# Kernel optimization log

Measured on AMD Instinct MI355X. Metric: run time of the kernel, lower is better.

The kernel has to match this reference:

```python
import jax, jax.numpy as jnp
import numpy as np

B, N_PER_G, H, K, A, GNN_STEPS = 64, 100, 64, 5, 50, 3
N = B * N_PER_G  # total nodes


def _lin(key, din, dout):
    s = 1.0 / np.sqrt(din)
    kw, kb = jax.random.split(key)
    w = jax.random.uniform(kw, (din, dout), minval=-s, maxval=s, dtype=jnp.float32)
    b = jax.random.uniform(kb, (dout,), minval=-s, maxval=s, dtype=jnp.float32)
    return w, b


def setup_inputs() -> dict:
    key = jax.random.key(0)
    ks = jax.random.split(key, 16)
    # complete graph (no self loops) per batch graph
    i, j = np.meshgrid(np.arange(N_PER_G), np.arange(N_PER_G), indexing="ij")
    m = i != j
    s0, d0 = i[m], j[m]  # [n*(n-1)]
    offs = (np.arange(B) * N_PER_G)[:, None]
    src = jnp.asarray((s0[None, :] + offs).reshape(-1), dtype=jnp.int32)
    dst = jnp.asarray((d0[None, :] + offs).reshape(-1), dtype=jnp.int32)
    E = src.shape[0]
    e_type = jax.random.uniform(ks[0], (E, 2), dtype=jnp.float32)
    d = jax.random.uniform(ks[1], (E, 1), dtype=jnp.float32)
    label = jax.nn.one_hot(jax.random.randint(ks[2], (N,), 0, K), K, dtype=jnp.float32)
    actions = jax.random.randint(ks[3], (B * A, 2), 0, N_PER_G)
    l1_w, l1_b = _lin(ks[4], K, H)
    l2_w, l2_b = _lin(ks[5], H, H)
    t3_w, t3_b = _lin(ks[6], H, H)
    t4_wf, t4_b = _lin(ks[7], 1, H)
    t5_wf, t5_b = _lin(ks[8], H, 1)
    t6_w, t6_b = _lin(ks[9], H, H)
    t7_1_w, t7_1_b = _lin(ks[10], H, H)
    t7_2_w, t7_2_b = _lin(ks[11], H, H)
    t9_1_w, t9_1_b = _lin(ks[12], H, H)
    t9_2_w, t9_2_b = _lin(ks[13], H, H)
    return dict(label=label, e_type=e_type, d=d,
                l1_w=l1_w, l1_b=l1_b, l2_w=l2_w, l2_b=l2_b,
                t3_w=t3_w, t3_b=t3_b, t4_w=t4_wf[0], t4_b=t4_b,
                t5_w=t5_wf[:, 0], t5_b=t5_b, t6_w=t6_w, t6_b=t6_b,
                t7_1_w=t7_1_w, t7_1_b=t7_1_b, t7_2_w=t7_2_w, t7_2_b=t7_2_b,
                t9_1_w=t9_1_w, t9_1_b=t9_1_b, t9_2_w=t9_2_w, t9_2_b=t9_2_b,
                src=src, dst=dst, actions=actions)


def reference(label, e_type, d, l1_w, l1_b, l2_w, l2_b, t3_w, t3_b, t4_w, t4_b,
              t5_w, t5_b, t6_w, t6_b, t7_1_w, t7_1_b, t7_2_w, t7_2_b,
              t9_1_w, t9_1_b, t9_2_w, t9_2_b, src, dst, actions):
    e1 = e_type[:, 0]
    # n1_hd = h[src]*e1, n1_d = d*e1; bmm(n1_hd^T, n1_d) == sum over in-edges of h[src]*e1^2*d
    w_e = (e1 * e1) * d[:, 0]                              # [E]
    s_e = d[:, 0] * e1                                     # per-edge n1_d scalar [E]
    # sum_deg relu(t4(n1_d)) as edge-parallel relu + scatter-add
    t4_edge = jax.nn.relu(s_e[:, None] * t4_w[None, :] + t4_b)   # [E,H]
    t4_sum = jax.ops.segment_sum(t4_edge, dst, num_segments=N)   # [N,H]
    base = label @ l1_w + l1_b + t4_sum @ t3_w + t3_b            # constant across gnn steps
    h = jnp.zeros((N, H), dtype=label.dtype)
    for _ in range(GNN_STEPS):
        n1_h = jax.ops.segment_sum(h[src] * w_e[:, None], dst, num_segments=N)  # [N,H]
        h = jax.nn.relu(base + n1_h @ l2_w + l2_b)
    # readout (forward_): graph mean -> t6 stem; per-action node-pair branch
    stem = h.reshape(B, N_PER_G, H).mean(axis=1) @ t6_w + t6_b    # [B,H]
    h2 = h @ t7_1_w + t7_1_b                                      # [N,H]
    offs = jnp.repeat(jnp.arange(B, dtype=actions.dtype) * N_PER_G, A)
    a = actions + offs[:, None]                                   # global node ids [B*A,2]
    ha = h2[a[:, 0]] + h2[a[:, 1]]                                # [B*A,H]
    u = jax.nn.relu(jax.nn.relu(ha) @ t7_2_w + t7_2_b) @ t9_2_w + t9_2_b
    g_branch = jax.nn.relu(stem) @ t9_1_w + t9_1_b                # [B,H]
    q = jax.nn.relu(g_branch[:, None, :] + u.reshape(B, A, H))    # [B,A,H]
    Q_sa = q.reshape(B * A, H) @ t5_w + t5_b[0]                   # [B*A]
    return Q_sa
```

## Files before the change

kernel.cpp:

```cpp
#include <hip/hip_runtime.h>

#define HD 64
#define NPG 100
#define NGRP 64
#define NACT 50
#define EPG 9900

typedef const float* fcp;

__global__ __launch_bounds__(512)
void k_edge_base(fcp label, fcp e_type, fcp dvec,
                 fcp l1_w, fcp l1_b, fcp l2_b,
                 fcp t3_w, fcp t3_b, fcp t4_w, fcp t4_b,
                 float* __restrict__ Wt, float* __restrict__ baseo,
                 float* __restrict__ hA)
{
    const int g  = blockIdx.x >> 2;
    const int c  = blockIdx.x & 3;
    const int j0 = c * 25;
    const int t  = threadIdx.x;
    const int hh = t & 63;
    const int w  = t >> 6;

    __shared__ __align__(16) float s_ld[2500];
    __shared__ __align__(16) float w_ld[2500];
    __shared__ __align__(16) float t4s[25 * HD];

    float lab[4][5], l1r[5];
    #pragma unroll
    for (int kk = 0; kk < 5; ++kk) l1r[kk] = l1_w[kk * HD + hh];
    #pragma unroll
    for (int m = 0; m < 4; ++m) {
        const int jl = w + 8 * m;
        #pragma unroll
        for (int kk = 0; kk < 5; ++kk)
            lab[m][kk] = (jl < 25) ? label[(g * NPG + j0 + jl) * 5 + kk] : 0.f;
    }

    const float2* et2 = (const float2*)e_type;
    const int ebase = g * EPG;
    for (int idx = t; idx < 2500; idx += 512) {
        const int i  = idx / 25;
        const int jl = idx - i * 25;
        const int j  = j0 + jl;
        float s = 0.f, wv = 0.f;
        if (i != j) {
            const int e = ebase + i * 99 + j - (j > i ? 1 : 0);
            const float e1 = et2[e].x;
            const float dd = dvec[e];
            s  = dd * e1;
            wv = e1 * e1 * dd;
        }
        s_ld[jl * 100 + i] = s;
        w_ld[jl * 100 + i] = wv;
    }
    __syncthreads();

    {
        float* wd = Wt + g * (NPG * NPG) + j0 * NPG;
        for (int idx = t; idx < 2500; idx += 512) wd[idx] = w_ld[idx];
    }

    const float w4  = t4_w[hh];
    const float b4  = t4_b[hh];
    const float rb4 = fmaxf(b4, 0.f);
    #pragma unroll
    for (int m = 0; m < 4; ++m) {
        const int jl = w + 8 * m;
        if (jl < 25) {
            float a0 = 0.f, a1 = 0.f, a2 = 0.f, a3 = 0.f;
            #pragma unroll 5
            for (int ib = 0; ib < 25; ++ib) {
                const float4 s4 = *(const float4*)&s_ld[jl * 100 + 4 * ib];
                a0 += fmaxf(s4.x * w4 + b4, 0.f);
                a1 += fmaxf(s4.y * w4 + b4, 0.f);
                a2 += fmaxf(s4.z * w4 + b4, 0.f);
                a3 += fmaxf(s4.w * w4 + b4, 0.f);
            }
            t4s[jl * HD + hh] = (a0 + a1) + (a2 + a3) - rb4;
        }
    }

    const float bb   = l1_b[hh] + t3_b[hh];
    const float l2bv = l2_b[hh];
    float v[4];
    #pragma unroll
    for (int m = 0; m < 4; ++m) {
        float x = bb;
        #pragma unroll
        for (int kk = 0; kk < 5; ++kk) x += lab[m][kk] * l1r[kk];
        v[m] = x;
    }
    for (int ib = 0; ib < 16; ++ib) {
        const float tw0 = t3_w[(4 * ib + 0) * HD + hh];
        const float tw1 = t3_w[(4 * ib + 1) * HD + hh];
        const float tw2 = t3_w[(4 * ib + 2) * HD + hh];
        const float tw3 = t3_w[(4 * ib + 3) * HD + hh];
        #pragma unroll
        for (int m = 0; m < 4; ++m) {
            const int jl = w + 8 * m;
            if (jl < 25) {
                const float4 x4 = *(const float4*)&t4s[jl * HD + 4 * ib];
                v[m] += x4.x * tw0 + x4.y * tw1 + x4.z * tw2 + x4.w * tw3;
            }
        }
    }
    #pragma unroll
    for (int m = 0; m < 4; ++m) {
        const int jl = w + 8 * m;
        if (jl < 25) {
            const int n = g * NPG + j0 + jl;
            baseo[n * HD + hh] = v[m];
            hA[n * HD + hh]    = fmaxf(v[m] + l2bv, 0.f);
        }
    }
}

__global__ __launch_bounds__(512)
void k_gnn_step(const float* __restrict__ Wt, const float* __restrict__ baseo,
                const float* __restrict__ h_old, fcp l2_w, fcp l2_b,
                float* __restrict__ h_new)
{
    const int g  = blockIdx.x >> 2;
    const int c  = blockIdx.x & 3;
    const int j0 = c * 25;
    const int t  = threadIdx.x;
    const int hh = t & 63;
    const int w  = t >> 6;

    __shared__ __align__(16) float hs[NPG * HD];
    __shared__ __align__(16) float wr[2500];
    __shared__ __align__(16) float n1s[25 * HD];

    float bs[4];
    #pragma unroll
    for (int m = 0; m < 4; ++m) {
        const int jl = w + 8 * m;
        bs[m] = (jl < 25) ? baseo[(g * NPG + j0 + jl) * HD + hh] : 0.f;
    }

    {
        const float4* ho4 = (const float4*)(h_old + g * NPG * HD);
        float4* hs4 = (float4*)hs;
        for (int idx = t; idx < NPG * HD / 4; idx += 512) hs4[idx] = ho4[idx];
        const float* wsrc = Wt + g * (NPG * NPG) + j0 * NPG;
        for (int idx = t; idx < 2500; idx += 512) wr[idx] = wsrc[idx];
    }
    __syncthreads();

    float acc[4];
    #pragma unroll
    for (int m = 0; m < 4; ++m) acc[m] = 0.f;
    for (int ib = 0; ib < 25; ++ib) {
        const float h0 = hs[(4 * ib + 0) * HD + hh];
        const float h1 = hs[(4 * ib + 1) * HD + hh];
        const float h2 = hs[(4 * ib + 2) * HD + hh];
        const float h3 = hs[(4 * ib + 3) * HD + hh];
        #pragma unroll
        for (int m = 0; m < 4; ++m) {
            const int jl = w + 8 * m;
            if (jl < 25) {
                const float4 wv = *(const float4*)&wr[jl * 100 + 4 * ib];
                acc[m] += wv.x * h0 + wv.y * h1 + wv.z * h2 + wv.w * h3;
            }
        }
    }
    #pragma unroll
    for (int m = 0; m < 4; ++m) {
        const int jl = w + 8 * m;
        if (jl < 25) n1s[jl * HD + hh] = acc[m];
    }

    const float l2bv = l2_b[hh];
    float v[4];
    #pragma unroll
    for (int m = 0; m < 4; ++m) v[m] = bs[m] + l2bv;
    for (int ib = 0; ib < 16; ++ib) {
        const float w0 = l2_w[(4 * ib + 0) * HD + hh];
        const float w1 = l2_w[(4 * ib + 1) * HD + hh];
        const float w2 = l2_w[(4 * ib + 2) * HD + hh];
        const float w3 = l2_w[(4 * ib + 3) * HD + hh];
        #pragma unroll
        for (int m = 0; m < 4; ++m) {
            const int jl = w + 8 * m;
            if (jl < 25) {
                const float4 x4 = *(const float4*)&n1s[jl * HD + 4 * ib];
                v[m] += x4.x * w0 + x4.y * w1 + x4.z * w2 + x4.w * w3;
            }
        }
    }
    #pragma unroll
    for (int m = 0; m < 4; ++m) {
        const int jl = w + 8 * m;
        if (jl < 25) h_new[(g * NPG + j0 + jl) * HD + hh] = fmaxf(v[m], 0.f);
    }
}

__global__ __launch_bounds__(512)
void k_tail(const float* __restrict__ hfin, const int* __restrict__ actions,
            fcp t5_w, fcp t5_b, fcp t6_w, fcp t6_b,
            fcp t7_1_w, fcp t7_1_b, fcp t7_2_w, fcp t7_2_b,
            fcp t9_1_w, fcp t9_1_b, fcp t9_2_w, fcp t9_2_b,
            float* __restrict__ out)
{
    const int g    = blockIdx.x >> 1;
    const int half = blockIdx.x & 1;
    const int t    = threadIdx.x;
    const int hh   = t & 63;
    const int aw   = t >> 6;

    __shared__ __align__(16) float hsb[NPG * HD];
    __shared__ __align__(16) float hsum[25 * HD];
    __shared__ __align__(16) float r1s[25 * HD];
    __shared__ __align__(16) float awk[8 * HD];
    __shared__ float gbuf[HD];

    int a0r[4], a1r[4];
    #pragma unroll
    for (int m = 0; m < 4; ++m) {
        const int al = aw + 7 * m;
        a0r[m] = 0; a1r[m] = 0;
        if (aw < 7 && al < 25) {
            const int a = g * NACT + half * 25 + al;
            a0r[m] = actions[a * 2 + 0];
            a1r[m] = actions[a * 2 + 1];
        }
    }

    {
        const float4* hg4 = (const float4*)(hfin + g * NPG * HD);
        float4* hs4 = (float4*)hsb;
        for (int idx = t; idx < NPG * HD / 4; idx += 512) hs4[idx] = hg4[idx];
    }
    __syncthreads();

    {
        float m = 0.f;
        for (int j = aw; j < NPG; j += 8) m += hsb[j * HD + hh];
        awk[aw * HD + hh] = m;
    }
    #pragma unroll
    for (int m = 0; m < 4; ++m) {
        const int al = aw + 7 * m;
        if (aw < 7 && al < 25)
            hsum[al * HD + hh] = hsb[a0r[m] * HD + hh] + hsb[a1r[m] * HD + hh];
    }
    __syncthreads();

    if (aw == 7) {
        float ml = 0.f;
        #pragma unroll
        for (int ww = 0; ww < 8; ++ww) ml += awk[ww * HD + hh];
        ml *= (1.f / NPG);
        float s = t6_b[hh];
        #pragma unroll 8
        for (int q = 0; q < HD; ++q) s += __shfl(ml, q, 64) * t6_w[q * HD + hh];
        s = fmaxf(s, 0.f);
        float gb = t9_1_b[hh];
        #pragma unroll 8
        for (int q = 0; q < HD; ++q) gb += __shfl(s, q, 64) * t9_1_w[q * HD + hh];
        gbuf[hh] = gb;
    } else {
        const float b71 = 2.f * t7_1_b[hh];
        float r[4];
        #pragma unroll
        for (int m = 0; m < 4; ++m) r[m] = b71;
        for (int ib = 0; ib < 16; ++ib) {
            const float w0 = t7_1_w[(4 * ib + 0) * HD + hh];
            const float w1 = t7_1_w[(4 * ib + 1) * HD + hh];
            const float w2 = t7_1_w[(4 * ib + 2) * HD + hh];
            const float w3 = t7_1_w[(4 * ib + 3) * HD + hh];
            #pragma unroll
            for (int m = 0; m < 4; ++m) {
                const int al = aw + 7 * m;
                if (al < 25) {
                    const float4 x4 = *(const float4*)&hsum[al * HD + 4 * ib];
                    r[m] += x4.x * w0 + x4.y * w1 + x4.z * w2 + x4.w * w3;
                }
            }
        }
        #pragma unroll
        for (int m = 0; m < 4; ++m) {
            const int al = aw + 7 * m;
            if (al < 25) r1s[al * HD + hh] = fmaxf(r[m], 0.f);
        }
        const float b72 = t7_2_b[hh];
        #pragma unroll
        for (int m = 0; m < 4; ++m) r[m] = b72;
        for (int ib = 0; ib < 16; ++ib) {
            const float w0 = t7_2_w[(4 * ib + 0) * HD + hh];
            const float w1 = t7_2_w[(4 * ib + 1) * HD + hh];
            const float w2 = t7_2_w[(4 * ib + 2) * HD + hh];
            const float w3 = t7_2_w[(4 * ib + 3) * HD + hh];
            #pragma unroll
            for (int m = 0; m < 4; ++m) {
                const int al = aw + 7 * m;
                if (al < 25) {
                    const float4 x4 = *(const float4*)&r1s[al * HD + 4 * ib];
                    r[m] += x4.x * w0 + x4.y * w1 + x4.z * w2 + x4.w * w3;
                }
            }
        }
        #pragma unroll
        for (int m = 0; m < 4; ++m) {
            const int al = aw + 7 * m;
            if (al < 25) hsum[al * HD + hh] = fmaxf(r[m], 0.f);
        }
    }
    __syncthreads();

    if (aw < 7) {
        const float b92  = t9_2_b[hh];
        const float t5wv = t5_w[hh];
        const float t5bv = t5_b[0];
        const float gbv  = gbuf[hh];
        float u[4];
        #pragma unroll
        for (int m = 0; m < 4; ++m) u[m] = b92;
        for (int ib = 0; ib < 16; ++ib) {
            const float w0 = t9_2_w[(4 * ib + 0) * HD + hh];
            const float w1 = t9_2_w[(4 * ib + 1) * HD + hh];
            const float w2 = t9_2_w[(4 * ib + 2) * HD + hh];
            const float w3 = t9_2_w[(4 * ib + 3) * HD + hh];
            #pragma unroll
            for (int m = 0; m < 4; ++m) {
                const int al = aw + 7 * m;
                if (al < 25) {
                    const float4 x4 = *(const float4*)&hsum[al * HD + 4 * ib];
                    u[m] += x4.x * w0 + x4.y * w1 + x4.z * w2 + x4.w * w3;
                }
            }
        }
        #pragma unroll
        for (int m = 0; m < 4; ++m) {
            const int al = aw + 7 * m;
            float qv = fmaxf(gbv + u[m], 0.f) * t5wv;
            #pragma unroll
            for (int off = 32; off > 0; off >>= 1) qv += __shfl_xor(qv, off, 64);
            if (al < 25 && hh == 0) out[g * NACT + half * 25 + al] = qv + t5bv;
        }
    }
}

extern "C" void kernel_launch(void* const* d_in, const int* in_sizes, int n_in,
                              void* d_out, int out_size, void* d_ws, size_t ws_size,
                              hipStream_t stream)
{
    fcp label  = (fcp)d_in[0];
    fcp e_type = (fcp)d_in[1];
    fcp dvec   = (fcp)d_in[2];
    fcp l1_w   = (fcp)d_in[3];
    fcp l1_b   = (fcp)d_in[4];
    fcp l2_w   = (fcp)d_in[5];
    fcp l2_b   = (fcp)d_in[6];
    fcp t3_w   = (fcp)d_in[7];
    fcp t3_b   = (fcp)d_in[8];
    fcp t4_w   = (fcp)d_in[9];
    fcp t4_b   = (fcp)d_in[10];
    fcp t5_w   = (fcp)d_in[11];
    fcp t5_b   = (fcp)d_in[12];
    fcp t6_w   = (fcp)d_in[13];
    fcp t6_b   = (fcp)d_in[14];
    fcp t7_1_w = (fcp)d_in[15];
    fcp t7_1_b = (fcp)d_in[16];
    fcp t7_2_w = (fcp)d_in[17];
    fcp t7_2_b = (fcp)d_in[18];
    fcp t9_1_w = (fcp)d_in[19];
    fcp t9_1_b = (fcp)d_in[20];
    fcp t9_2_w = (fcp)d_in[21];
    fcp t9_2_b = (fcp)d_in[22];
    const int* actions = (const int*)d_in[25];

    char* ws = (char*)d_ws;
    float* Wt   = (float*)(ws);
    float* base = (float*)(ws + 2560000);
    float* hA   = (float*)(ws + 2560000 + 1638400);
    float* hB   = (float*)(ws + 2560000 + 2 * 1638400);

    k_edge_base<<<dim3(NGRP * 4), dim3(512), 0, stream>>>(
        label, e_type, dvec, l1_w, l1_b, l2_b, t3_w, t3_b, t4_w, t4_b,
        Wt, base, hA);
    k_gnn_step<<<dim3(NGRP * 4), dim3(512), 0, stream>>>(Wt, base, hA, l2_w, l2_b, hB);
    k_gnn_step<<<dim3(NGRP * 4), dim3(512), 0, stream>>>(Wt, base, hB, l2_w, l2_b, hA);
    k_tail<<<dim3(NGRP * 2), dim3(512), 0, stream>>>(
        hA, actions, t5_w, t5_b, t6_w, t6_b, t7_1_w, t7_1_b, t7_2_w, t7_2_b,
        t9_1_w, t9_1_b, t9_2_w, t9_2_b, (float*)d_out);
}
```

Baseline: 171.0 us.

## Fuse edge, GNN steps, and readout into one kernel per graph

Replaces the four launches (edge/base, two GNN steps, tail) with one kernel that processes a whole graph per 1024-thread block. Node state, edge weights and intermediates stay in shared memory, so the global Wt/base/h workspace round-trips and the inter-kernel launch gaps go away. The cost is only 64 blocks on a many-CU GPU and heavy LDS use per block, which lowers parallelism.

```diff
diff --git a/kernel.cpp b/kernel.cpp
--- a/kernel.cpp
+++ b/kernel.cpp
@@ -8,249 +8,189 @@
 
 typedef const float* fcp;
 
-__global__ __launch_bounds__(512)
-void k_edge_base(fcp label, fcp e_type, fcp dvec,
-                 fcp l1_w, fcp l1_b, fcp l2_b,
-                 fcp t3_w, fcp t3_b, fcp t4_w, fcp t4_b,
-                 float* __restrict__ Wt, float* __restrict__ baseo,
-                 float* __restrict__ hA)
+__global__ __launch_bounds__(1024)
+void k_fused(fcp label, fcp e_type, fcp dvec,
+             fcp l1_w, fcp l1_b, fcp l2_w, fcp l2_b,
+             fcp t3_w, fcp t3_b, fcp t4_w, fcp t4_b,
+             fcp t5_w, fcp t5_b, fcp t6_w, fcp t6_b,
+             fcp t7_1_w, fcp t7_1_b, fcp t7_2_w, fcp t7_2_b,
+             fcp t9_1_w, fcp t9_1_b, fcp t9_2_w, fcp t9_2_b,
+             const int* __restrict__ actions,
+             float* __restrict__ out)
 {
-    const int g  = blockIdx.x >> 2;
-    const int c  = blockIdx.x & 3;
-    const int j0 = c * 25;
+    const int g  = blockIdx.x;
     const int t  = threadIdx.x;
     const int hh = t & 63;
     const int w  = t >> 6;
 
-    __shared__ __align__(16) float s_ld[2500];
-    __shared__ __align__(16) float w_ld[2500];
-    __shared__ __align__(16) float t4s[25 * HD];
-
-    float lab[4][5], l1r[5];
+    __shared__ __align__(16) float sh_h[NPG * HD];
+    __shared__ __align__(16) float sh_wt[NPG * NPG];
+    __shared__ __align__(16) float sh_s[NPG * NPG];
+    __shared__ __align__(16) float awk[16 * HD];
+    __shared__ float gbuf[HD];
+
+    float l1r[5];
     #pragma unroll
     for (int kk = 0; kk < 5; ++kk) l1r[kk] = l1_w[kk * HD + hh];
+
+    float basev[7];
+    #pragma unroll
+    for (int m = 0; m < 7; ++m) {
+        const int j = w + 16 * m;
+        float x = 0.f;
+        if (j < NPG) {
+            #pragma unroll
+            for (int kk = 0; kk < 5; ++kk)
+                x += label[(g * NPG + j) * 5 + kk] * l1r[kk];
+        }
+        basev[m] = x;
+    }
+
+    int a0r[4], a1r[4];
     #pragma unroll
     for (int m = 0; m < 4; ++m) {
-        const int jl = w + 8 * m;
-        #pragma unroll
-        for (int kk = 0; kk < 5; ++kk)
-            lab[m][kk] = (jl < 25) ? label[(g * NPG + j0 + jl) * 5 + kk] : 0.f;
-    }
-
-    const float2* et2 = (const float2*)e_type;
+        const int al = w + 15 * m;
+        a0r[m] = 0; a1r[m] = 0;
+        if (w < 15 && al < NACT) {
+            const int a = g * NACT + al;
+            a0r[m] = actions[a * 2 + 0];
+            a1r[m] = actions[a * 2 + 1];
+        }
+    }
+
     const int ebase = g * EPG;
-    for (int idx = t; idx < 2500; idx += 512) {
-        const int i  = idx / 25;
-        const int jl = idx - i * 25;
-        const int j  = j0 + jl;
+    for (int idx = t; idx < NPG * NPG; idx += 1024) {
+        const int i = idx / NPG;
+        const int j = idx - i * NPG;
         float s = 0.f, wv = 0.f;
         if (i != j) {
             const int e = ebase + i * 99 + j - (j > i ? 1 : 0);
-            const float e1 = et2[e].x;
+            const float e1 = e_type[2 * e];
             const float dd = dvec[e];
             s  = dd * e1;
             wv = e1 * e1 * dd;
         }
-        s_ld[jl * 100 + i] = s;
-        w_ld[jl * 100 + i] = wv;
+        sh_s[j * NPG + i]  = s;
+        sh_wt[j * NPG + i] = wv;
     }
     __syncthreads();
-
-    {
-        float* wd = Wt + g * (NPG * NPG) + j0 * NPG;
-        for (int idx = t; idx < 2500; idx += 512) wd[idx] = w_ld[idx];
-    }
 
     const float w4  = t4_w[hh];
     const float b4  = t4_b[hh];
     const float rb4 = fmaxf(b4, 0.f);
     #pragma unroll
-    for (int m = 0; m < 4; ++m) {
-        const int jl = w + 8 * m;
-        if (jl < 25) {
+    for (int m = 0; m < 7; ++m) {
+        const int j = w + 16 * m;
+        if (j < NPG) {
             float a0 = 0.f, a1 = 0.f, a2 = 0.f, a3 = 0.f;
             #pragma unroll 5
             for (int ib = 0; ib < 25; ++ib) {
-                const float4 s4 = *(const float4*)&s_ld[jl * 100 + 4 * ib];
+                const float4 s4 = *(const float4*)&sh_s[j * NPG + 4 * ib];
                 a0 += fmaxf(s4.x * w4 + b4, 0.f);
                 a1 += fmaxf(s4.y * w4 + b4, 0.f);
                 a2 += fmaxf(s4.z * w4 + b4, 0.f);
                 a3 += fmaxf(s4.w * w4 + b4, 0.f);
             }
-            t4s[jl * HD + hh] = (a0 + a1) + (a2 + a3) - rb4;
+            sh_h[j * HD + hh] = (a0 + a1) + (a2 + a3) - rb4;
         }
     }
 
     const float bb   = l1_b[hh] + t3_b[hh];
     const float l2bv = l2_b[hh];
-    float v[4];
-    #pragma unroll
-    for (int m = 0; m < 4; ++m) {
-        float x = bb;
-        #pragma unroll
-        for (int kk = 0; kk < 5; ++kk) x += lab[m][kk] * l1r[kk];
-        v[m] = x;
-    }
+    #pragma unroll
+    for (int m = 0; m < 7; ++m) basev[m] += bb;
     for (int ib = 0; ib < 16; ++ib) {
         const float tw0 = t3_w[(4 * ib + 0) * HD + hh];
         const float tw1 = t3_w[(4 * ib + 1) * HD + hh];
         const float tw2 = t3_w[(4 * ib + 2) * HD + hh];
         const float tw3 = t3_w[(4 * ib + 3) * HD + hh];
         #pragma unroll
+        for (int m = 0; m < 7; ++m) {
+            const int j = w + 16 * m;
+            if (j < NPG) {
+                const float4 x4 = *(const float4*)&sh_h[j * HD + 4 * ib];
+                basev[m] += x4.x * tw0 + x4.y * tw1 + x4.z * tw2 + x4.w * tw3;
+            }
+        }
+    }
+    #pragma unroll
+    for (int m = 0; m < 7; ++m) {
+        const int j = w + 16 * m;
+        if (j < NPG) sh_h[j * HD + hh] = fmaxf(basev[m] + l2bv, 0.f);
+    }
+    __syncthreads();
+
+    #pragma unroll 1
+    for (int step = 0; step < 2; ++step) {
+        float acc[7];
+        #pragma unroll
+        for (int m = 0; m < 7; ++m) acc[m] = 0.f;
+        for (int ib = 0; ib < 25; ++ib) {
+            const float h0 = sh_h[(4 * ib + 0) * HD + hh];
+            const float h1 = sh_h[(4 * ib + 1) * HD + hh];
+            const float h2 = sh_h[(4 * ib + 2) * HD + hh];
+            const float h3 = sh_h[(4 * ib + 3) * HD + hh];
+            #pragma unroll
+            for (int m = 0; m < 7; ++m) {
+                const int j = w + 16 * m;
+                if (j < NPG) {
+                    const float4 wv = *(const float4*)&sh_wt[j * NPG + 4 * ib];
+                    acc[m] += wv.x * h0 + wv.y * h1 + wv.z * h2 + wv.w * h3;
+                }
+            }
+        }
+        #pragma unroll
+        for (int m = 0; m < 7; ++m) {
+            const int j = w + 16 * m;
+            if (j < NPG) sh_s[j * HD + hh] = acc[m];
+        }
+        float v[7];
+        #pragma unroll
+        for (int m = 0; m < 7; ++m) v[m] = basev[m] + l2bv;
+        for (int ib = 0; ib < 16; ++ib) {
+            const float w0 = l2_w[(4 * ib + 0) * HD + hh];
+            const float w1 = l2_w[(4 * ib + 1) * HD + hh];
+            const float w2 = l2_w[(4 * ib + 2) * HD + hh];
+            const float w3 = l2_w[(4 * ib + 3) * HD + hh];
+            #pragma unroll
+            for (int m = 0; m < 7; ++m) {
+                const int j = w + 16 * m;
+                if (j < NPG) {
+                    const float4 x4 = *(const float4*)&sh_s[j * HD + 4 * ib];
+                    v[m] += x4.x * w0 + x4.y * w1 + x4.z * w2 + x4.w * w3;
+                }
+            }
+        }
+        __syncthreads();
+        #pragma unroll
+        for (int m = 0; m < 7; ++m) {
+            const int j = w + 16 * m;
+            if (j < NPG) sh_h[j * HD + hh] = fmaxf(v[m], 0.f);
+        }
+        __syncthreads();
+    }
+
+    {
+        float ml = 0.f;
+        for (int j = w; j < NPG; j += 16) ml += sh_h[j * HD + hh];
+        awk[w * HD + hh] = ml;
+    }
+    float* hsum = sh_s;
+    float* r1s  = sh_s + NACT * HD;
+    if (w < 15) {
+        #pragma unroll
         for (int m = 0; m < 4; ++m) {
-            const int jl = w + 8 * m;
-            if (jl < 25) {
-                const float4 x4 = *(const float4*)&t4s[jl * HD + 4 * ib];
-                v[m] += x4.x * tw0 + x4.y * tw1 + x4.z * tw2 + x4.w * tw3;
-            }
-        }
-    }
-    #pragma unroll
-    for (int m = 0; m < 4; ++m) {
-        const int jl = w + 8 * m;
-        if (jl < 25) {
-            const int n = g * NPG + j0 + jl;
-            baseo[n * HD + hh] = v[m];
-            hA[n * HD + hh]    = fmaxf(v[m] + l2bv, 0.f);
-        }
-    }
-}
-
-__global__ __launch_bounds__(512)
-void k_gnn_step(const float* __restrict__ Wt, const float* __restrict__ baseo,
-                const float* __restrict__ h_old, fcp l2_w, fcp l2_b,
-                float* __restrict__ h_new)
-{
-    const int g  = blockIdx.x >> 2;
-    const int c  = blockIdx.x & 3;
-    const int j0 = c * 25;
-    const int t  = threadIdx.x;
-    const int hh = t & 63;
-    const int w  = t >> 6;
-
-    __shared__ __align__(16) float hs[NPG * HD];
-    __shared__ __align__(16) float wr[2500];
-    __shared__ __align__(16) float n1s[25 * HD];
-
-    float bs[4];
-    #pragma unroll
-    for (int m = 0; m < 4; ++m) {
-        const int jl = w + 8 * m;
-        bs[m] = (jl < 25) ? baseo[(g * NPG + j0 + jl) * HD + hh] : 0.f;
-    }
-
-    {
-        const float4* ho4 = (const float4*)(h_old + g * NPG * HD);
-        float4* hs4 = (float4*)hs;
-        for (int idx = t; idx < NPG * HD / 4; idx += 512) hs4[idx] = ho4[idx];
-        const float* wsrc = Wt + g * (NPG * NPG) + j0 * NPG;
-        for (int idx = t; idx < 2500; idx += 512) wr[idx] = wsrc[idx];
+            const int al = w + 15 * m;
+            if (al < NACT)
+                hsum[al * HD + hh] = sh_h[a0r[m] * HD + hh] + sh_h[a1r[m] * HD + hh];
+        }
     }
     __syncthreads();
 
-    float acc[4];
-    #pragma unroll
-    for (int m = 0; m < 4; ++m) acc[m] = 0.f;
-    for (int ib = 0; ib < 25; ++ib) {
-        const float h0 = hs[(4 * ib + 0) * HD + hh];
-        const float h1 = hs[(4 * ib + 1) * HD + hh];
-        const float h2 = hs[(4 * ib + 2) * HD + hh];
-        const float h3 = hs[(4 * ib + 3) * HD + hh];
-        #pragma unroll
-        for (int m = 0; m < 4; ++m) {
-            const int jl = w + 8 * m;
-            if (jl < 25) {
-                const float4 wv = *(const float4*)&wr[jl * 100 + 4 * ib];
-                acc[m] += wv.x * h0 + wv.y * h1 + wv.z * h2 + wv.w * h3;
-            }
-        }
-    }
-    #pragma unroll
-    for (int m = 0; m < 4; ++m) {
-        const int jl = w + 8 * m;
-        if (jl < 25) n1s[jl * HD + hh] = acc[m];
-    }
-
-    const float l2bv = l2_b[hh];
-    float v[4];
-    #pragma unroll
-    for (int m = 0; m < 4; ++m) v[m] = bs[m] + l2bv;
-    for (int ib = 0; ib < 16; ++ib) {
-        const float w0 = l2_w[(4 * ib + 0) * HD + hh];
-        const float w1 = l2_w[(4 * ib + 1) * HD + hh];
-        const float w2 = l2_w[(4 * ib + 2) * HD + hh];
-        const float w3 = l2_w[(4 * ib + 3) * HD + hh];
-        #pragma unroll
-        for (int m = 0; m < 4; ++m) {
-            const int jl = w + 8 * m;
-            if (jl < 25) {
-                const float4 x4 = *(const float4*)&n1s[jl * HD + 4 * ib];
-                v[m] += x4.x * w0 + x4.y * w1 + x4.z * w2 + x4.w * w3;
-            }
-        }
-    }
-    #pragma unroll
-    for (int m = 0; m < 4; ++m) {
-        const int jl = w + 8 * m;
-        if (jl < 25) h_new[(g * NPG + j0 + jl) * HD + hh] = fmaxf(v[m], 0.f);
-    }
-}
-
-__global__ __launch_bounds__(512)
-void k_tail(const float* __restrict__ hfin, const int* __restrict__ actions,
-            fcp t5_w, fcp t5_b, fcp t6_w, fcp t6_b,
-            fcp t7_1_w, fcp t7_1_b, fcp t7_2_w, fcp t7_2_b,
-            fcp t9_1_w, fcp t9_1_b, fcp t9_2_w, fcp t9_2_b,
-            float* __restrict__ out)
-{
-    const int g    = blockIdx.x >> 1;
-    const int half = blockIdx.x & 1;
-    const int t    = threadIdx.x;
-    const int hh   = t & 63;
-    const int aw   = t >> 6;
-
-    __shared__ __align__(16) float hsb[NPG * HD];
-    __shared__ __align__(16) float hsum[25 * HD];
-    __shared__ __align__(16) float r1s[25 * HD];
-    __shared__ __align__(16) float awk[8 * HD];
-    __shared__ float gbuf[HD];
-
-    int a0r[4], a1r[4];
-    #pragma unroll
-    for (int m = 0; m < 4; ++m) {
-        const int al = aw + 7 * m;
-        a0r[m] = 0; a1r[m] = 0;
-        if (aw < 7 && al < 25) {
-            const int a = g * NACT + half * 25 + al;
-            a0r[m] = actions[a * 2 + 0];
-            a1r[m] = actions[a * 2 + 1];
-        }
-    }
-
-    {
-        const float4* hg4 = (const float4*)(hfin + g * NPG * HD);
-        float4* hs4 = (float4*)hsb;
-        for (int idx = t; idx < NPG * HD / 4; idx += 512) hs4[idx] = hg4[idx];
-    }
-    __syncthreads();
-
-    {
-        float m = 0.f;
-        for (int j = aw; j < NPG; j += 8) m += hsb[j * HD + hh];
-        awk[aw * HD + hh] = m;
-    }
-    #pragma unroll
-    for (int m = 0; m < 4; ++m) {
-        const int al = aw + 7 * m;
-        if (aw < 7 && al < 25)
-            hsum[al * HD + hh] = hsb[a0r[m] * HD + hh] + hsb[a1r[m] * HD + hh];
-    }
-    __syncthreads();
-
-    if (aw == 7) {
+    if (w == 15) {
         float ml = 0.f;
         #pragma unroll
-        for (int ww = 0; ww < 8; ++ww) ml += awk[ww * HD + hh];
+        for (int ww = 0; ww < 16; ++ww) ml += awk[ww * HD + hh];
         ml *= (1.f / NPG);
         float s = t6_b[hh];
         #pragma unroll 8
@@ -272,8 +212,8 @@
             const float w3 = t7_1_w[(4 * ib + 3) * HD + hh];
             #pragma unroll
             for (int m = 0; m < 4; ++m) {
-                const int al = aw + 7 * m;
-                if (al < 25) {
+                const int al = w + 15 * m;
+                if (al < NACT) {
                     const float4 x4 = *(const float4*)&hsum[al * HD + 4 * ib];
                     r[m] += x4.x * w0 + x4.y * w1 + x4.z * w2 + x4.w * w3;
                 }
@@ -281,8 +221,8 @@
         }
         #pragma unroll
         for (int m = 0; m < 4; ++m) {
-            const int al = aw + 7 * m;
-            if (al < 25) r1s[al * HD + hh] = fmaxf(r[m], 0.f);
+            const int al = w + 15 * m;
+            if (al < NACT) r1s[al * HD + hh] = fmaxf(r[m], 0.f);
         }
         const float b72 = t7_2_b[hh];
         #pragma unroll
@@ -294,8 +234,8 @@
             const float w3 = t7_2_w[(4 * ib + 3) * HD + hh];
             #pragma unroll
             for (int m = 0; m < 4; ++m) {
-                const int al = aw + 7 * m;
-                if (al < 25) {
+                const int al = w + 15 * m;
+                if (al < NACT) {
                     const float4 x4 = *(const float4*)&r1s[al * HD + 4 * ib];
                     r[m] += x4.x * w0 + x4.y * w1 + x4.z * w2 + x4.w * w3;
                 }
@@ -303,13 +243,13 @@
         }
         #pragma unroll
         for (int m = 0; m < 4; ++m) {
-            const int al = aw + 7 * m;
-            if (al < 25) hsum[al * HD + hh] = fmaxf(r[m], 0.f);
+            const int al = w + 15 * m;
+            if (al < NACT) hsum[al * HD + hh] = fmaxf(r[m], 0.f);
         }
     }
     __syncthreads();
 
-    if (aw < 7) {
+    if (w < 15) {
         const float b92  = t9_2_b[hh];
         const float t5wv = t5_w[hh];
         const float t5bv = t5_b[0];
@@ -324,8 +264,8 @@
             const float w3 = t9_2_w[(4 * ib + 3) * HD + hh];
             #pragma unroll
             for (int m = 0; m < 4; ++m) {
-                const int al = aw + 7 * m;
-                if (al < 25) {
+                const int al = w + 15 * m;
+                if (al < NACT) {
                     const float4 x4 = *(const float4*)&hsum[al * HD + 4 * ib];
                     u[m] += x4.x * w0 + x4.y * w1 + x4.z * w2 + x4.w * w3;
                 }
@@ -333,11 +273,11 @@
         }
         #pragma unroll
         for (int m = 0; m < 4; ++m) {
-            const int al = aw + 7 * m;
+            const int al = w + 15 * m;
             float qv = fmaxf(gbv + u[m], 0.f) * t5wv;
             #pragma unroll
             for (int off = 32; off > 0; off >>= 1) qv += __shfl_xor(qv, off, 64);
-            if (al < 25 && hh == 0) out[g * NACT + half * 25 + al] = qv + t5bv;
+            if (al < NACT && hh == 0) out[g * NACT + al] = qv + t5bv;
         }
     }
 }
@@ -371,18 +311,8 @@
     fcp t9_2_b = (fcp)d_in[22];
     const int* actions = (const int*)d_in[25];
 
-    char* ws = (char*)d_ws;
-    float* Wt   = (float*)(ws);
-    float* base = (float*)(ws + 2560000);
-    float* hA   = (float*)(ws + 2560000 + 1638400);
-    float* hB   = (float*)(ws + 2560000 + 2 * 1638400);
-
-    k_edge_base<<<dim3(NGRP * 4), dim3(512), 0, stream>>>(
-        label, e_type, dvec, l1_w, l1_b, l2_b, t3_w, t3_b, t4_w, t4_b,
-        Wt, base, hA);
-    k_gnn_step<<<dim3(NGRP * 4), dim3(512), 0, stream>>>(Wt, base, hA, l2_w, l2_b, hB);
-    k_gnn_step<<<dim3(NGRP * 4), dim3(512), 0, stream>>>(Wt, base, hB, l2_w, l2_b, hA);
-    k_tail<<<dim3(NGRP * 2), dim3(512), 0, stream>>>(
-        hA, actions, t5_w, t5_b, t6_w, t6_b, t7_1_w, t7_1_b, t7_2_w, t7_2_b,
-        t9_1_w, t9_1_b, t9_2_w, t9_2_b, (float*)d_out);
+    k_fused<<<dim3(NGRP), dim3(1024), 0, stream>>>(
+        label, e_type, dvec, l1_w, l1_b, l2_w, l2_b, t3_w, t3_b, t4_w, t4_b,
+        t5_w, t5_b, t6_w, t6_b, t7_1_w, t7_1_b, t7_2_w, t7_2_b,
+        t9_1_w, t9_1_b, t9_2_w, t9_2_b, actions, (float*)d_out);
 }
```

Measured after the change: 184.2 us. +7.7%, slower.
